# Optimization experiments

Hardware: AMD Instinct MI355X
Metric: run time of the kernel (lower is better)

The kernel has to match this reference:

```python
import jax, jax.numpy as jnp
import numpy as np

B, S, K = 128, 196, 512   # batch, encoder seq, keys_hidden_size
T_CAP = 16                # caption length (out_seq_len = 15)
V, E, H = 32000, 512, 512 # vocab, embedding, hidden


def setup_inputs() -> dict:
    key = jax.random.key(0)
    ks = jax.random.split(key, 16)
    sc = lambda fan_in: 1.0 / np.sqrt(fan_in)
    return {
        "features": jax.random.normal(ks[0], (B, S, K), jnp.float32),
        "captions": jax.random.randint(ks[1], (B, T_CAP), 0, V),
        "emb": jax.random.normal(ks[2], (V, E), jnp.float32) * 0.02,
        "fc1_w": jax.random.normal(ks[3], (H, E), jnp.float32) * sc(E),
        "fc1_b": jnp.zeros((H,), jnp.float32),
        "att_wq": jax.random.normal(ks[4], (H, H), jnp.float32) * sc(H),
        "att_wk": jax.random.normal(ks[5], (H, K), jnp.float32) * sc(K),
        "att_v": jax.random.normal(ks[6], (H,), jnp.float32) * sc(H),
        "fc0_w": jax.random.normal(ks[7], (H, K), jnp.float32) * sc(K),
        "fc0_b": jnp.zeros((H,), jnp.float32),
        "gru_wih": jax.random.normal(ks[8], (3 * H, 2 * H), jnp.float32) * sc(2 * H),
        "gru_whh": jax.random.normal(ks[9], (3 * H, H), jnp.float32) * sc(H),
        "gru_bih": jnp.zeros((3 * H,), jnp.float32),
        "gru_bhh": jnp.zeros((3 * H,), jnp.float32),
        "fc2_w": jax.random.normal(ks[10], (V, H), jnp.float32) * sc(H),
        "fc2_b": jnp.zeros((V,), jnp.float32),
    }


def reference(features, captions, emb, fc1_w, fc1_b, att_wq, att_wk, att_v,
              fc0_w, fc0_b, gru_wih, gru_whh, gru_bih, gru_bhh, fc2_w, fc2_b):
    # embed captions and project: (B, T_CAP, H)
    x = emb[captions] @ fc1_w.T + fc1_b
    # precompute key projection for Bahdanau attention: (B, S, H)
    keys_proj = features @ att_wk.T

    def step(h, x_t):
        # Bahdanau additive attention
        q = h @ att_wq.T                                   # (B, H)
        scores = jnp.tanh(q[:, None, :] + keys_proj) @ att_v  # (B, S)
        w = jax.nn.softmax(scores, axis=1)
        context = jnp.einsum('bs,bsk->bk', w, features)    # (B, K)
        context = context @ fc0_w.T + fc0_b                # fc_0 -> (B, H)
        rnn_in = jnp.concatenate([x_t, context], axis=-1)  # (B, 2H)
        # GRU cell, torch gate order (r, z, n)
        gi = rnn_in @ gru_wih.T + gru_bih
        gh = h @ gru_whh.T + gru_bhh
        ir, iz, inn = jnp.split(gi, 3, axis=-1)
        hr, hz, hn = jnp.split(gh, 3, axis=-1)
        r = jax.nn.sigmoid(ir + hr)
        z = jax.nn.sigmoid(iz + hz)
        n = jnp.tanh(inn + r * hn)
        h_new = (1.0 - z) * n + z * h
        out = h_new @ fc2_w.T + fc2_b                      # fc_2 -> (B, V)
        return h_new, out

    out_seq_len = captions.shape[1] - 1
    xs = jnp.swapaxes(x[:, :out_seq_len], 0, 1)            # (T, B, H)
    h0 = jnp.zeros((features.shape[0], fc0_b.shape[0]), features.dtype)
    _, outs = jax.lax.scan(step, h0, xs)                   # (T, B, V)
    return jnp.swapaxes(outs, 0, 1)                        # (B, T, V)
```

## Files before the change

kernel.cpp:

```cpp
#include <hip/hip_runtime.h>

typedef _Float16 half_t;
typedef float    floatx4 __attribute__((ext_vector_type(4)));
typedef _Float16 halfx8  __attribute__((ext_vector_type(8)));
typedef _Float16 halfx2  __attribute__((ext_vector_type(2)));

__device__ __forceinline__ float tanh_f(float x) {
  float e = __expf(2.0f * x);
  return 1.0f - 2.0f / (e + 1.0f);
}
__device__ __forceinline__ float sigmoid_f(float x) {
  return 1.0f / (1.0f + __expf(-x));
}

__device__ __forceinline__ void gl16(const void* g, void* s) {
  __builtin_amdgcn_global_load_lds((__attribute__((address_space(1))) unsigned int*)g,
                                   (__attribute__((address_space(3))) unsigned int*)s,
                                   16, 0, 0);
}

__global__ __launch_bounds__(256) void k_cvt_f16(const float* __restrict__ src,
                                                 half_t* __restrict__ dst, int n) {
  int i = (blockIdx.x * 256 + threadIdx.x) * 4;
  if (i < n) {
    float4 v = *(const float4*)(src + i);
    halfx2 a; a[0] = (half_t)v.x; a[1] = (half_t)v.y;
    halfx2 b; b[0] = (half_t)v.z; b[1] = (half_t)v.w;
    *(halfx2*)(dst + i) = a;
    *(halfx2*)(dst + i + 2) = b;
  }
}

__global__ __launch_bounds__(256) void k_wihsplit(const float* __restrict__ wih,
                                                  half_t* __restrict__ wx,
                                                  half_t* __restrict__ wc) {
  int row = blockIdx.x, j = threadIdx.x * 2;
  float2 a = *(const float2*)(wih + (size_t)row * 1024 + j);
  float2 b = *(const float2*)(wih + (size_t)row * 1024 + 512 + j);
  halfx2 ax; ax[0] = (half_t)a.x; ax[1] = (half_t)a.y;
  halfx2 bx; bx[0] = (half_t)b.x; bx[1] = (half_t)b.y;
  *(halfx2*)(wx + (size_t)row * 512 + j) = ax;
  *(halfx2*)(wc + (size_t)row * 512 + j) = bx;
}

__global__ __launch_bounds__(256) void k_gather(const float* __restrict__ emb,
                                                const int* __restrict__ cap,
                                                half_t* __restrict__ dst) {
  int row = blockIdx.x;
  int b = row / 15, t = row - b * 15;
  int c = cap[b * 16 + t];
  const float* s = emb + (size_t)c * 512;
  int e = threadIdx.x * 2;
  float2 v = *(const float2*)(s + e);
  halfx2 o; o[0] = (half_t)v.x; o[1] = (half_t)v.y;
  *(halfx2*)(dst + (size_t)row * 512 + e) = o;
}

__global__ __launch_bounds__(256) void k_biasc(const float* __restrict__ fc0b,
                                               float* __restrict__ biasc) {
  int i = blockIdx.x * 256 + threadIdx.x;
  biasc[i] = (i < 512) ? 0.f : fc0b[i - 512];
}

__global__ __launch_bounds__(256) void k_zero(float4* p) {
  p[blockIdx.x * 256 + threadIdx.x] = make_float4(0.f, 0.f, 0.f, 0.f);
}

template <bool A_F32, bool OUT_F16>
__device__ __forceinline__ void gemm128_body(const void* __restrict__ Ap,
                                             const half_t* __restrict__ Bp,
                                             const float* __restrict__ bias,
                                             void* __restrict__ Cp,
                                             const int Kd, const int ldc,
                                             const int m0, const int n0) {
  constexpr int ABYTES = A_F32 ? (128 * 32 * 4) : (128 * 32 * 2);
  constexpr int BBYTES = 128 * 32 * 2;
  __shared__ __align__(16) char smem[2 * ABYTES + 2 * BBYTES];

  const int l = threadIdx.x & 63;
  const int w = threadIdx.x >> 6;

  const float*  gAf = nullptr;
  const half_t* gAh = nullptr;
  if constexpr (A_F32) {
    gAf = (const float*)Ap + (size_t)(m0 + w * 32 + (l >> 3)) * Kd + (l & 7) * 4;
  } else {
    gAh = (const half_t*)Ap + (size_t)(m0 + w * 32 + (l >> 2)) * Kd + (l & 3) * 8;
  }
  const half_t* gB = Bp + (size_t)(n0 + w * 32 + (l >> 2)) * Kd + (l & 3) * 8;

  const int fr = l & 15;
  const int kq = (l >> 4) * 8;
  const int mh = (w & 1) * 64;
  const int nh = (w >> 1) * 64;

  floatx4 acc[4][4];
#pragma unroll
  for (int i = 0; i < 4; ++i)
#pragma unroll
    for (int j = 0; j < 4; ++j) { floatx4 z = {0.f, 0.f, 0.f, 0.f}; acc[i][j] = z; }

  const int NT = Kd >> 5;

  auto stage = [&](int tt) {
    const int k0 = tt * 32;
    char* aD = smem + (tt & 1) * ABYTES;
    char* bD = smem + 2 * ABYTES + (tt & 1) * BBYTES;
    if constexpr (A_F32) {
      const float* g = gAf + k0;
#pragma unroll
      for (int j = 0; j < 4; ++j)
        gl16(g + (size_t)j * 8 * Kd, aD + (w * 32 + j * 8) * 128);
    } else {
      const half_t* g = gAh + k0;
      gl16(g, aD + (w * 32) * 64);
      gl16(g + (size_t)16 * Kd, aD + (w * 32 + 16) * 64);
    }
    const half_t* g2 = gB + k0;
    gl16(g2, bD + (w * 32) * 64);
    gl16(g2 + (size_t)16 * Kd, bD + (w * 32 + 16) * 64);
  };

  stage(0);

  for (int t = 0; t < NT; ++t) {
    __syncthreads();
    if (t + 1 < NT) stage(t + 1);
    const char* aB = smem + (t & 1) * ABYTES;
    const char* bB = smem + 2 * ABYTES + (t & 1) * BBYTES;
    halfx8 af[4], bf[4];
#pragma unroll
    for (int i = 0; i < 4; ++i) {
      if constexpr (A_F32) {
        const float* la = (const float*)aB + (size_t)(mh + i * 16 + fr) * 32 + kq;
        float4 v0 = *(const float4*)la;
        float4 v1 = *(const float4*)(la + 4);
        halfx8 a;
        a[0] = (half_t)v0.x; a[1] = (half_t)v0.y; a[2] = (half_t)v0.z; a[3] = (half_t)v0.w;
        a[4] = (half_t)v1.x; a[5] = (half_t)v1.y; a[6] = (half_t)v1.z; a[7] = (half_t)v1.w;
        af[i] = a;
      } else {
        af[i] = *(const halfx8*)((const half_t*)aB + (size_t)(mh + i * 16 + fr) * 32 + kq);
      }
      bf[i] = *(const halfx8*)((const half_t*)bB + (size_t)(nh + i * 16 + fr) * 32 + kq);
    }
#pragma unroll
    for (int i = 0; i < 4; ++i)
#pragma unroll
      for (int j = 0; j < 4; ++j)
        acc[i][j] = __builtin_amdgcn_mfma_f32_16x16x32_f16(af[i], bf[j], acc[i][j], 0, 0, 0);
  }

#pragma unroll
  for (int j = 0; j < 4; ++j) {
    const int n = n0 + nh + j * 16 + fr;
    const float bv = bias ? bias[n] : 0.0f;
#pragma unroll
    for (int i = 0; i < 4; ++i) {
      const int mb = m0 + mh + i * 16 + (l >> 4) * 4;
#pragma unroll
      for (int r = 0; r < 4; ++r) {
        const float v = acc[i][j][r] + bv;
        const size_t ci = (size_t)(mb + r) * ldc + n;
        if constexpr (OUT_F16) ((half_t*)Cp)[ci] = (half_t)v;
        else                   ((float*)Cp)[ci] = v;
      }
    }
  }
}

template <bool A_F32, bool OUT_F16>
__global__ __launch_bounds__(256) void k_gemm_lds(const void* __restrict__ Ap,
                                                  const half_t* __restrict__ Bp,
                                                  const float* __restrict__ bias,
                                                  void* __restrict__ Cp,
                                                  int Kd, int ldc) {
  gemm128_body<A_F32, OUT_F16>(Ap, Bp, bias, Cp, Kd, ldc,
                               blockIdx.y * 128, blockIdx.x * 128);
}

__global__ __launch_bounds__(256) void k_fc2gru_lds(const half_t* __restrict__ hh,
                                                    const half_t* __restrict__ fc2w,
                                                    const float* __restrict__ fc2b,
                                                    const half_t* __restrict__ bcat2,
                                                    float* __restrict__ outp,
                                                    float* __restrict__ ghq) {
  const bool isfc2 = blockIdx.x < 250;
  const half_t* B = isfc2 ? fc2w : bcat2;
  const float* bias = isfc2 ? fc2b : nullptr;
  void* C = isfc2 ? (void*)outp : (void*)ghq;
  const int ldc = isfc2 ? 480000 : 2048;
  const int n0 = (isfc2 ? blockIdx.x : (blockIdx.x - 250)) * 128;
  gemm128_body<false, false>(hh, B, bias, C, 512, ldc, 0, n0);
}

__global__ __launch_bounds__(256) void k_scores(const half_t* __restrict__ kpfp,
                                                const float* __restrict__ ghq,
                                                const float* __restrict__ attv,
                                                float* __restrict__ scores) {
  int w = blockIdx.x * 4 + (threadIdx.x >> 6);
  int l = threadIdx.x & 63;
  int b = w / 196;
  halfx8 kv = *(const halfx8*)(kpfp + (size_t)w * 1024 + l * 8);
  const float* qr = ghq + (size_t)b * 2048 + 1536 + l * 8;
  float4 q0 = *(const float4*)qr;
  float4 q1 = *(const float4*)(qr + 4);
  float4 a0 = *(const float4*)(attv + l * 8);
  float4 a1 = *(const float4*)(attv + l * 8 + 4);
  float acc = a0.x * tanh_f(q0.x + (float)kv[0]);
  acc += a0.y * tanh_f(q0.y + (float)kv[1]);
  acc += a0.z * tanh_f(q0.z + (float)kv[2]);
  acc += a0.w * tanh_f(q0.w + (float)kv[3]);
  acc += a1.x * tanh_f(q1.x + (float)kv[4]);
  acc += a1.y * tanh_f(q1.y + (float)kv[5]);
  acc += a1.z * tanh_f(q1.z + (float)kv[6]);
  acc += a1.w * tanh_f(q1.w + (float)kv[7]);
#pragma unroll
  for (int off = 32; off > 0; off >>= 1) acc += __shfl_xor(acc, off, 64);
  if (l == 0) scores[w] = acc;
}

__global__ __launch_bounds__(256) void k_ctx(const float* __restrict__ scores,
                                             const half_t* __restrict__ kpfp,
                                             half_t* __restrict__ ctxo) {
  const int b = blockIdx.x, kt = blockIdx.y * 128, t = threadIdx.x;
  __shared__ float sw[196], red[256];
  float sc = (t < 196) ? scores[b * 196 + t] : -1e30f;
  red[t] = sc; __syncthreads();
  for (int o = 128; o > 0; o >>= 1) { if (t < o) red[t] = fmaxf(red[t], red[t + o]); __syncthreads(); }
  float mx = red[0]; __syncthreads();
  float e = (t < 196) ? __expf(sc - mx) : 0.f;
  red[t] = e; __syncthreads();
  for (int o = 128; o > 0; o >>= 1) { if (t < o) red[t] += red[t + o]; __syncthreads(); }
  float inv = 1.0f / red[0];
  if (t < 196) sw[t] = e * inv;
  __syncthreads();
  const int kk = t & 127, half = t >> 7, s0 = half * 98;
  const half_t* fp = kpfp + (size_t)(b * 196 + s0) * 1024 + 512 + kt + kk;
  float acc = 0.f;
#pragma unroll 7
  for (int i = 0; i < 98; ++i) acc += sw[s0 + i] * (float)fp[(size_t)i * 1024];
  red[t] = acc; __syncthreads();
  if (t < 128) ctxo[(size_t)b * 512 + kt + t] = (half_t)(red[t] + red[t + 128]);
}

__global__ __launch_bounds__(256) void k_gates(const float* __restrict__ gix,
                                               const float* __restrict__ gic,
                                               const float* __restrict__ ghq,
                                               const float* __restrict__ bih,
                                               const float* __restrict__ bhh,
                                               float* __restrict__ hbuf,
                                               half_t* __restrict__ hh, int step) {
  int idx = blockIdx.x * 256 + threadIdx.x;
  int b = idx >> 9, n = idx & 511;
  const float* gx = gix + (size_t)(b * 15 + step) * 1536;
  const float* gc = gic + (size_t)b * 1536;
  const float* gh = ghq + (size_t)b * 2048;
  float ir  = gx[n]        + gc[n]        + bih[n];
  float iz  = gx[n + 512]  + gc[n + 512]  + bih[n + 512];
  float in_ = gx[n + 1024] + gc[n + 1024] + bih[n + 1024];
  float hr  = gh[n]        + bhh[n];
  float hz  = gh[n + 512]  + bhh[n + 512];
  float hn  = gh[n + 1024] + bhh[n + 1024];
  float r = sigmoid_f(ir + hr);
  float z = sigmoid_f(iz + hz);
  float nn = tanh_f(in_ + r * hn);
  float hv = (1.0f - z) * nn + z * hbuf[idx];
  hbuf[idx] = hv;
  hh[idx] = (half_t)hv;
}

extern "C" void kernel_launch(void* const* d_in, const int* in_sizes, int n_in,
                              void* d_out, int out_size, void* d_ws, size_t ws_size,
                              hipStream_t stream) {
  (void)in_sizes; (void)n_in; (void)out_size; (void)ws_size;
  const float* features = (const float*)d_in[0];
  const int*   captions = (const int*)d_in[1];
  const float* emb      = (const float*)d_in[2];
  const float* fc1_w    = (const float*)d_in[3];
  const float* fc1_b    = (const float*)d_in[4];
  const float* att_wq   = (const float*)d_in[5];
  const float* att_wk   = (const float*)d_in[6];
  const float* att_v    = (const float*)d_in[7];
  const float* fc0_w    = (const float*)d_in[8];
  const float* fc0_b    = (const float*)d_in[9];
  const float* gru_wih  = (const float*)d_in[10];
  const float* gru_whh  = (const float*)d_in[11];
  const float* gru_bih  = (const float*)d_in[12];
  const float* gru_bhh  = (const float*)d_in[13];
  const float* fc2_w    = (const float*)d_in[14];
  const float* fc2_b    = (const float*)d_in[15];
  float* out = (float*)d_out;

  char* p = (char*)d_ws;
  half_t* kpfp   = (half_t*)p; p += (size_t)25088 * 1024 * 2;
  half_t* fc2w_h = (half_t*)p; p += (size_t)32000 * 512 * 2;
  float*  gix    = (float*)p;  p += (size_t)1920 * 1536 * 4;
  half_t* wihx_h = (half_t*)p; p += (size_t)1536 * 512 * 2;
  half_t* wihc_h = (half_t*)p; p += (size_t)1536 * 512 * 2;
  half_t* bcat2  = (half_t*)p; p += (size_t)2048 * 512 * 2;
  half_t* wkfc0  = (half_t*)p; p += (size_t)1024 * 512 * 2;
  half_t* fc1w_h = (half_t*)p; p += (size_t)512 * 512 * 2;
  half_t* embg_h = (half_t*)p; p += (size_t)1920 * 512 * 2;
  half_t* xproj_h= (half_t*)p; p += (size_t)1920 * 512 * 2;
  float*  biasc  = (float*)p;  p += (size_t)1024 * 4;
  float*  ghq    = (float*)p;  p += (size_t)128 * 2048 * 4;
  float*  hbuf   = (float*)p;  p += (size_t)128 * 512 * 4;
  float*  scores = (float*)p;  p += (size_t)128 * 196 * 4;
  float*  gic    = (float*)p;  p += (size_t)128 * 1536 * 4;
  half_t* ctxo   = (half_t*)p; p += (size_t)128 * 512 * 2;
  half_t* h_h    = (half_t*)p; p += (size_t)128 * 512 * 2;

  k_cvt_f16<<<dim3(16000), 256, 0, stream>>>(fc2_w, fc2w_h, 32000 * 512);
  k_cvt_f16<<<dim3(256),   256, 0, stream>>>(fc1_w, fc1w_h, 512 * 512);
  k_cvt_f16<<<dim3(256),   256, 0, stream>>>(att_wk, wkfc0, 512 * 512);
  k_cvt_f16<<<dim3(256),   256, 0, stream>>>(fc0_w, wkfc0 + (size_t)512 * 512, 512 * 512);
  k_cvt_f16<<<dim3(768),   256, 0, stream>>>(gru_whh, bcat2, 1536 * 512);
  k_cvt_f16<<<dim3(256),   256, 0, stream>>>(att_wq, bcat2 + (size_t)1536 * 512, 512 * 512);
  k_wihsplit<<<dim3(1536), 256, 0, stream>>>(gru_wih, wihx_h, wihc_h);
  k_gather<<<dim3(1920), 256, 0, stream>>>(emb, captions, embg_h);
  k_biasc<<<dim3(4), 256, 0, stream>>>(fc0_b, biasc);
  k_zero<<<dim3(320), 256, 0, stream>>>((float4*)ghq);
  k_gemm_lds<false, true><<<dim3(4, 15), 256, 0, stream>>>(embg_h, fc1w_h, fc1_b, xproj_h, 512, 512);
  k_gemm_lds<true, true><<<dim3(8, 196), 256, 0, stream>>>(features, wkfc0, biasc, kpfp, 512, 1024);
  k_gemm_lds<false, false><<<dim3(12, 15), 256, 0, stream>>>(xproj_h, wihx_h, nullptr, gix, 512, 1536);

  for (int t = 0; t < 15; ++t) {
    k_scores<<<dim3(6272), 256, 0, stream>>>(kpfp, ghq, att_v, scores);
    k_ctx<<<dim3(128, 4), 256, 0, stream>>>(scores, kpfp, ctxo);
    k_gemm_lds<false, false><<<dim3(12, 1), 256, 0, stream>>>(ctxo, wihc_h, nullptr, gic, 512, 1536);
    k_gates<<<dim3(256), 256, 0, stream>>>(gix, gic, ghq, gru_bih, gru_bhh, hbuf, h_h, t);
    k_fc2gru_lds<<<dim3(266), 256, 0, stream>>>(h_h, fc2w_h, fc2_b, bcat2, out + (size_t)t * 32000, ghq);
  }
}
```

Measured before the change: 1.221 ms.

## Hoist fc2 out of recurrence into one batched GEMM over all timesteps

The vocab projection no longer runs inside each of the 15 recurrent steps as a narrow M=128 GEMM. Each step's hidden state is now stored into a history buffer, and a single large GEMM over all 1920 rows runs after the loop, launched with an XCD-aware block swizzle. The per-step launch keeps only the recurrent GEMM (gh plus q). Features are pre-converted to fp16 so the key-projection GEMM uses the fp16 path, and that GEMM also gets its own block remap. The aim is to reread the fc2 weights far less often and to fill the GPU better, at the cost of an extra conversion pass and more workspace.

```diff
diff --git a/kernel.cpp b/kernel.cpp
--- a/kernel.cpp
+++ b/kernel.cpp
@@ -17,6 +17,11 @@
   __builtin_amdgcn_global_load_lds((__attribute__((address_space(1))) unsigned int*)g,
                                    (__attribute__((address_space(3))) unsigned int*)s,
                                    16, 0, 0);
+}
+
+__device__ __forceinline__ int xcd_swz(int bid, int nwg) {
+  int q = nwg >> 3, r = nwg & 7, x = bid & 7, p = bid >> 3;
+  return (x < r ? x * (q + 1) : r * (q + 1) + (x - r) * q) + p;
 }
 
 __global__ __launch_bounds__(256) void k_cvt_f16(const float* __restrict__ src,
@@ -66,27 +71,21 @@
   p[blockIdx.x * 256 + threadIdx.x] = make_float4(0.f, 0.f, 0.f, 0.f);
 }
 
-template <bool A_F32, bool OUT_F16>
-__device__ __forceinline__ void gemm128_body(const void* __restrict__ Ap,
+template <bool OUT_F16>
+__device__ __forceinline__ void gemm128_body(const half_t* __restrict__ Ap,
                                              const half_t* __restrict__ Bp,
                                              const float* __restrict__ bias,
                                              void* __restrict__ Cp,
                                              const int Kd, const int ldc,
                                              const int m0, const int n0) {
-  constexpr int ABYTES = A_F32 ? (128 * 32 * 4) : (128 * 32 * 2);
+  constexpr int ABYTES = 128 * 32 * 2;
   constexpr int BBYTES = 128 * 32 * 2;
   __shared__ __align__(16) char smem[2 * ABYTES + 2 * BBYTES];
 
   const int l = threadIdx.x & 63;
   const int w = threadIdx.x >> 6;
 
-  const float*  gAf = nullptr;
-  const half_t* gAh = nullptr;
-  if constexpr (A_F32) {
-    gAf = (const float*)Ap + (size_t)(m0 + w * 32 + (l >> 3)) * Kd + (l & 7) * 4;
-  } else {
-    gAh = (const half_t*)Ap + (size_t)(m0 + w * 32 + (l >> 2)) * Kd + (l & 3) * 8;
-  }
+  const half_t* gA = Ap + (size_t)(m0 + w * 32 + (l >> 2)) * Kd + (l & 3) * 8;
   const half_t* gB = Bp + (size_t)(n0 + w * 32 + (l >> 2)) * Kd + (l & 3) * 8;
 
   const int fr = l & 15;
@@ -106,16 +105,9 @@
     const int k0 = tt * 32;
     char* aD = smem + (tt & 1) * ABYTES;
     char* bD = smem + 2 * ABYTES + (tt & 1) * BBYTES;
-    if constexpr (A_F32) {
-      const float* g = gAf + k0;
-#pragma unroll
-      for (int j = 0; j < 4; ++j)
-        gl16(g + (size_t)j * 8 * Kd, aD + (w * 32 + j * 8) * 128);
-    } else {
-      const half_t* g = gAh + k0;
-      gl16(g, aD + (w * 32) * 64);
-      gl16(g + (size_t)16 * Kd, aD + (w * 32 + 16) * 64);
-    }
+    const half_t* g = gA + k0;
+    gl16(g, aD + (w * 32) * 64);
+    gl16(g + (size_t)16 * Kd, aD + (w * 32 + 16) * 64);
     const half_t* g2 = gB + k0;
     gl16(g2, bD + (w * 32) * 64);
     gl16(g2 + (size_t)16 * Kd, bD + (w * 32 + 16) * 64);
@@ -131,17 +123,7 @@
     halfx8 af[4], bf[4];
 #pragma unroll
     for (int i = 0; i < 4; ++i) {
-      if constexpr (A_F32) {
-        const float* la = (const float*)aB + (size_t)(mh + i * 16 + fr) * 32 + kq;
-        float4 v0 = *(const float4*)la;
-        float4 v1 = *(const float4*)(la + 4);
-        halfx8 a;
-        a[0] = (half_t)v0.x; a[1] = (half_t)v0.y; a[2] = (half_t)v0.z; a[3] = (half_t)v0.w;
-        a[4] = (half_t)v1.x; a[5] = (half_t)v1.y; a[6] = (half_t)v1.z; a[7] = (half_t)v1.w;
-        af[i] = a;
-      } else {
-        af[i] = *(const halfx8*)((const half_t*)aB + (size_t)(mh + i * 16 + fr) * 32 + kq);
-      }
+      af[i] = *(const halfx8*)((const half_t*)aB + (size_t)(mh + i * 16 + fr) * 32 + kq);
       bf[i] = *(const halfx8*)((const half_t*)bB + (size_t)(nh + i * 16 + fr) * 32 + kq);
     }
 #pragma unroll
@@ -169,29 +151,34 @@
   }
 }
 
-template <bool A_F32, bool OUT_F16>
-__global__ __launch_bounds__(256) void k_gemm_lds(const void* __restrict__ Ap,
+template <bool OUT_F16>
+__global__ __launch_bounds__(256) void k_gemm_lds(const half_t* __restrict__ Ap,
                                                   const half_t* __restrict__ Bp,
                                                   const float* __restrict__ bias,
                                                   void* __restrict__ Cp,
                                                   int Kd, int ldc) {
-  gemm128_body<A_F32, OUT_F16>(Ap, Bp, bias, Cp, Kd, ldc,
-                               blockIdx.y * 128, blockIdx.x * 128);
-}
-
-__global__ __launch_bounds__(256) void k_fc2gru_lds(const half_t* __restrict__ hh,
-                                                    const half_t* __restrict__ fc2w,
-                                                    const float* __restrict__ fc2b,
-                                                    const half_t* __restrict__ bcat2,
-                                                    float* __restrict__ outp,
-                                                    float* __restrict__ ghq) {
-  const bool isfc2 = blockIdx.x < 250;
-  const half_t* B = isfc2 ? fc2w : bcat2;
-  const float* bias = isfc2 ? fc2b : nullptr;
-  void* C = isfc2 ? (void*)outp : (void*)ghq;
-  const int ldc = isfc2 ? 480000 : 2048;
-  const int n0 = (isfc2 ? blockIdx.x : (blockIdx.x - 250)) * 128;
-  gemm128_body<false, false>(hh, B, bias, C, 512, ldc, 0, n0);
+  gemm128_body<OUT_F16>(Ap, Bp, bias, Cp, Kd, ldc,
+                        blockIdx.y * 128, blockIdx.x * 128);
+}
+
+__global__ __launch_bounds__(256) void k_kpfp(const half_t* __restrict__ featf,
+                                              const half_t* __restrict__ wkfc0,
+                                              const float* __restrict__ biasc,
+                                              half_t* __restrict__ kpfp) {
+  const int w = (blockIdx.x & 7) * 196 + (blockIdx.x >> 3);
+  const int n0 = (w & 7) * 128;
+  const int m0 = (w >> 3) * 128;
+  gemm128_body<true>(featf, wkfc0, biasc, kpfp, 512, 1024, m0, n0);
+}
+
+__global__ __launch_bounds__(256) void k_fc2_final(const half_t* __restrict__ hall,
+                                                   const half_t* __restrict__ fc2w,
+                                                   const float* __restrict__ fc2b,
+                                                   float* __restrict__ outp) {
+  const int w = xcd_swz(blockIdx.x, 3750);
+  const int m0 = (w % 15) * 128;
+  const int n0 = (w / 15) * 128;
+  gemm128_body<false>(hall, fc2w, fc2b, outp, 512, 32000, m0, n0);
 }
 
 __global__ __launch_bounds__(256) void k_scores(const half_t* __restrict__ kpfp,
@@ -250,7 +237,8 @@
                                                const float* __restrict__ bih,
                                                const float* __restrict__ bhh,
                                                float* __restrict__ hbuf,
-                                               half_t* __restrict__ hh, int step) {
+                                               half_t* __restrict__ hh,
+                                               half_t* __restrict__ hall, int step) {
   int idx = blockIdx.x * 256 + threadIdx.x;
   int b = idx >> 9, n = idx & 511;
   const float* gx = gix + (size_t)(b * 15 + step) * 1536;
@@ -267,7 +255,9 @@
   float nn = tanh_f(in_ + r * hn);
   float hv = (1.0f - z) * nn + z * hbuf[idx];
   hbuf[idx] = hv;
-  hh[idx] = (half_t)hv;
+  half_t h16 = (half_t)hv;
+  hh[idx] = h16;
+  hall[(size_t)(b * 15 + step) * 512 + n] = h16;
 }
 
 extern "C" void kernel_launch(void* const* d_in, const int* in_sizes, int n_in,
@@ -310,8 +300,11 @@
   float*  gic    = (float*)p;  p += (size_t)128 * 1536 * 4;
   half_t* ctxo   = (half_t*)p; p += (size_t)128 * 512 * 2;
   half_t* h_h    = (half_t*)p; p += (size_t)128 * 512 * 2;
+  half_t* featf  = (half_t*)p; p += (size_t)25088 * 512 * 2;
+  half_t* hall   = (half_t*)p; p += (size_t)1920 * 512 * 2;
 
   k_cvt_f16<<<dim3(16000), 256, 0, stream>>>(fc2_w, fc2w_h, 32000 * 512);
+  k_cvt_f16<<<dim3(12544), 256, 0, stream>>>(features, featf, 25088 * 512);
   k_cvt_f16<<<dim3(256),   256, 0, stream>>>(fc1_w, fc1w_h, 512 * 512);
   k_cvt_f16<<<dim3(256),   256, 0, stream>>>(att_wk, wkfc0, 512 * 512);
   k_cvt_f16<<<dim3(256),   256, 0, stream>>>(fc0_w, wkfc0 + (size_t)512 * 512, 512 * 512);
@@ -321,15 +314,16 @@
   k_gather<<<dim3(1920), 256, 0, stream>>>(emb, captions, embg_h);
   k_biasc<<<dim3(4), 256, 0, stream>>>(fc0_b, biasc);
   k_zero<<<dim3(320), 256, 0, stream>>>((float4*)ghq);
-  k_gemm_lds<false, true><<<dim3(4, 15), 256, 0, stream>>>(embg_h, fc1w_h, fc1_b, xproj_h, 512, 512);
-  k_gemm_lds<true, true><<<dim3(8, 196), 256, 0, stream>>>(features, wkfc0, biasc, kpfp, 512, 1024);
-  k_gemm_lds<false, false><<<dim3(12, 15), 256, 0, stream>>>(xproj_h, wihx_h, nullptr, gix, 512, 1536);
+  k_gemm_lds<true><<<dim3(4, 15), 256, 0, stream>>>(embg_h, fc1w_h, fc1_b, xproj_h, 512, 512);
+  k_kpfp<<<dim3(1568), 256, 0, stream>>>(featf, wkfc0, biasc, kpfp);
+  k_gemm_lds<false><<<dim3(12, 15), 256, 0, stream>>>(xproj_h, wihx_h, nullptr, gix, 512, 1536);
 
   for (int t = 0; t < 15; ++t) {
     k_scores<<<dim3(6272), 256, 0, stream>>>(kpfp, ghq, att_v, scores);
     k_ctx<<<dim3(128, 4), 256, 0, stream>>>(scores, kpfp, ctxo);
-    k_gemm_lds<false, false><<<dim3(12, 1), 256, 0, stream>>>(ctxo, wihc_h, nullptr, gic, 512, 1536);
-    k_gates<<<dim3(256), 256, 0, stream>>>(gix, gic, ghq, gru_bih, gru_bhh, hbuf, h_h, t);
-    k_fc2gru_lds<<<dim3(266), 256, 0, stream>>>(h_h, fc2w_h, fc2_b, bcat2, out + (size_t)t * 32000, ghq);
+    k_gemm_lds<false><<<dim3(12, 1), 256, 0, stream>>>(ctxo, wihc_h, nullptr, gic, 512, 1536);
+    k_gates<<<dim3(256), 256, 0, stream>>>(gix, gic, ghq, gru_bih, gru_bhh, hbuf, h_h, hall, t);
+    k_gemm_lds<false><<<dim3(16, 1), 256, 0, stream>>>(h_h, bcat2, nullptr, ghq, 512, 2048);
   }
-}
+  k_fc2_final<<<dim3(3750), 256, 0, stream>>>(hall, fc2w_h, fc2_b, out);
+}
```

Result: no change. 1.206 ms (-1.2%).
